# Optimization experiments

Measured on AMD Instinct MI355X. Metric: run time of the kernel, lower is better.

Reference implementation:

```python
import jax, jax.numpy as jnp
import numpy as np

NEG_INF = -9.0e15
ALPHA = 0.2  # leakyrelu slope


def setup_inputs() -> dict:
    key = jax.random.key(0)
    k1, k2, k3, k4, k5 = jax.random.split(key, 5)
    B, N, D_IN, D_OUT = 8, 2048, 128, 128
    h = jax.random.normal(k1, (B, N, D_IN), dtype=jnp.float32)
    adj = jax.random.randint(k2, (N, N), 0, 2, dtype=jnp.int32)
    W = jax.random.normal(k3, (D_IN, D_OUT), dtype=jnp.float32) * (1.0 / np.sqrt(D_IN))
    a_src = jax.random.normal(k4, (D_OUT,), dtype=jnp.float32) * (1.0 / np.sqrt(D_OUT))
    a_dst = jax.random.normal(k5, (D_OUT,), dtype=jnp.float32) * (1.0 / np.sqrt(D_OUT))
    return {"h": h, "adj": adj, "W": W, "a_src": a_src, "a_dst": a_dst}


def reference(h, adj, W, a_src, a_dst):
    # Wh: [B, N, D_out]
    Wh = jnp.einsum("bnd,de->bne", h, W)
    e_src = jnp.einsum("bne,e->bn", Wh, a_src)  # [B, N]
    e_dst = jnp.einsum("bne,e->bn", Wh, a_dst)  # [B, N]
    # additive attention logits: e[b,i,j] = e_src[b,i] + e_dst[b,j]
    e = e_src[:, :, None] + e_dst[:, None, :]  # [B, N, N]
    e = jnp.where(e > 0, e, ALPHA * e)  # leaky relu
    e = jnp.where(adj[None, :, :] > 0, e, NEG_INF)
    attention = jax.nn.softmax(e, axis=-1)  # [B, N, N]
    h_prime = jnp.einsum("bij,bje->bie", attention, Wh)
    return h_prime
```

## Files before the change

kernel.cpp:

```cpp
#include <hip/hip_runtime.h>
#include <stdint.h>

#define ALPHA 0.2f
#define LOG2E 1.4426950408889634f

typedef unsigned short u16;
typedef short s16x8 __attribute__((ext_vector_type(8)));
typedef float f32x4 __attribute__((ext_vector_type(4)));

union BF8 { s16x8 v; uint32_t u[4]; u16 s[8]; uint4 q; };

static __device__ __forceinline__ float bf2f(u16 u) {
  union { uint32_t i; float f; } c; c.i = ((uint32_t)u) << 16; return c.f;
}
static __device__ __forceinline__ uint32_t pk2bf(float lo, float hi) {
  uint32_t ul = __float_as_uint(lo) + 0x8000u;
  uint32_t uh = __float_as_uint(hi) + 0x8000u;
  return (ul >> 16) | (uh & 0xffff0000u);
}

static __device__ __forceinline__ void gl2lds16(const void* g, void* l) {
  __builtin_amdgcn_global_load_lds(
      (const __attribute__((address_space(1))) uint32_t*)g,
      (__attribute__((address_space(3))) uint32_t*)l, 16, 0, 0);
}

__global__ __launch_bounds__(256) void k_zero(uint32_t* __restrict__ out, int n32) {
  int gid = blockIdx.x * 256 + threadIdx.x;
  if (gid < n32) out[gid] = 0u;
}

__global__ __launch_bounds__(256) void k_pack_adj(const int* __restrict__ adj,
                                                  uint32_t* __restrict__ bits,
                                                  const u16* __restrict__ h,
                                                  int* __restrict__ flag) {
  int tid = threadIdx.x;
  int base = blockIdx.x * 256 + tid;
#pragma unroll
  for (int it = 0; it < 8; ++it) {
    int gid = base + it * (2048 * 256);
    unsigned long long m = __ballot(adj[gid] != 0);
    if ((tid & 63) == 0)
      *(unsigned long long*)(&bits[gid >> 5]) = m;
  }
  if (blockIdx.x == 0 && tid < 64) {
    u16 v = h[2 * tid];
    int e = (v >> 7) & 0xff;
    unsigned long long dm = __ballot(e >= 100 && e <= 140);
    if (tid == 0) flag[0] = (__popcll(dm) >= 48) ? 1 : 0;
  }
}

__global__ __launch_bounds__(256) void k_wh(
    const void* __restrict__ hV, const void* __restrict__ WgV,
    const void* __restrict__ aSrcV, const void* __restrict__ aDstV,
    const int* __restrict__ flag,
    u16* __restrict__ WhT, float* __restrict__ eS, float* __restrict__ eD) {
  __shared__ __align__(16) char smemRaw[34816];
  u16*   WT   = (u16*)smemRaw;
  float* tile = (float*)smemRaw;
  __shared__ float aS[128], aD[128];

  const int tid = threadIdx.x;
  const int mb = blockIdx.x * 64;
  const int isBf = *flag;

  if (isBf) {
    const u16* Wg = (const u16*)WgV;
    for (int it = 0; it < 8; ++it) {
      int idx = tid + it * 256;
      int k = idx >> 4, c0 = (idx & 15) * 8;
      uint4 w4 = *(const uint4*)(Wg + (k << 7) + c0);
      u16* wsv = (u16*)&w4;
#pragma unroll
      for (int e = 0; e < 8; ++e) WT[(c0 + e) * 136 + k] = wsv[e];
    }
    if (tid < 128) aS[tid] = bf2f(((const u16*)aSrcV)[tid]);
    else           aD[tid - 128] = bf2f(((const u16*)aDstV)[tid - 128]);
  } else {
    const float* Wg = (const float*)WgV;
    for (int it = 0; it < 8; ++it) {
      int idx = tid + it * 256;
      int k = idx >> 4, c0 = (idx & 15) * 8;
      float4 w0 = *(const float4*)(Wg + (k << 7) + c0);
      float4 w1 = *(const float4*)(Wg + (k << 7) + c0 + 4);
      float wf[8] = {w0.x, w0.y, w0.z, w0.w, w1.x, w1.y, w1.z, w1.w};
#pragma unroll
      for (int e = 0; e < 8; ++e)
        WT[(c0 + e) * 136 + k] = (u16)((__float_as_uint(wf[e]) + 0x8000u) >> 16);
    }
    if (tid < 128) aS[tid] = ((const float*)aSrcV)[tid];
    else           aD[tid - 128] = ((const float*)aDstV)[tid - 128];
  }
  __syncthreads();

  const int wv = tid >> 6, lane = tid & 63, ln = lane & 15, quad = lane >> 4;
  const int row = mb + wv * 16 + ln;

  f32x4 acc[8];
#pragma unroll
  for (int t = 0; t < 8; ++t) acc[t] = (f32x4){0.f, 0.f, 0.f, 0.f};

  if (isBf) {
    const u16* h = (const u16*)hV;
#pragma unroll
    for (int ks = 0; ks < 4; ++ks) {
      s16x8 af = *(const s16x8*)(h + (row << 7) + ks * 32 + quad * 8);
#pragma unroll
      for (int t = 0; t < 8; ++t) {
        s16x8 bfg = *(const s16x8*)(&WT[(t * 16 + ln) * 136 + ks * 32 + quad * 8]);
        acc[t] = __builtin_amdgcn_mfma_f32_16x16x32_bf16(af, bfg, acc[t], 0, 0, 0);
      }
    }
  } else {
    const float* h = (const float*)hV;
#pragma unroll
    for (int ks = 0; ks < 4; ++ks) {
      float4 a0 = *(const float4*)(h + (row << 7) + ks * 32 + quad * 8);
      float4 a1 = *(const float4*)(h + (row << 7) + ks * 32 + quad * 8 + 4);
      BF8 af;
      af.u[0] = pk2bf(a0.x, a0.y);
      af.u[1] = pk2bf(a0.z, a0.w);
      af.u[2] = pk2bf(a1.x, a1.y);
      af.u[3] = pk2bf(a1.z, a1.w);
#pragma unroll
      for (int t = 0; t < 8; ++t) {
        s16x8 bfg = *(const s16x8*)(&WT[(t * 16 + ln) * 136 + ks * 32 + quad * 8]);
        acc[t] = __builtin_amdgcn_mfma_f32_16x16x32_bf16(af.v, bfg, acc[t], 0, 0, 0);
      }
    }
  }
  __syncthreads();

#pragma unroll
  for (int t = 0; t < 8; ++t)
#pragma unroll
    for (int r = 0; r < 4; ++r)
      tile[(wv * 16 + quad * 4 + r) * 130 + t * 16 + ln] = acc[t][r];
  __syncthreads();

  if (tid < 128) {
    int r = tid & 63, grp = tid >> 6;
    const float* a = grp ? aD : aS;
    float sum = 0.f;
#pragma unroll 4
    for (int d = 0; d < 128; ++d) sum += tile[r * 130 + d] * a[d];
    int m = mb + r, b = m >> 11, n = m & 2047;
    (grp ? eD : eS)[(b << 11) + n] = sum * LOG2E;
  }

  {
    int d = tid >> 1, half = tid & 1;
    int n0 = mb & 2047, b = mb >> 11;
    uint32_t pk[16];
#pragma unroll
    for (int qq = 0; qq < 16; ++qq) {
      float v0 = tile[(half * 32 + 2 * qq) * 130 + d];
      float v1 = tile[(half * 32 + 2 * qq + 1) * 130 + d];
      pk[qq] = pk2bf(v0, v1);
    }
    uint4* dst = (uint4*)(WhT + (size_t)((b << 7) + d) * 2048 + n0 + half * 32);
#pragma unroll
    for (int c = 0; c < 4; ++c)
      dst[c] = make_uint4(pk[c * 4], pk[c * 4 + 1], pk[c * 4 + 2], pk[c * 4 + 3]);
  }
}

__global__ __launch_bounds__(512, 8) void k_attn(
    const u16* __restrict__ WhT, const float* __restrict__ eSrc,
    const float* __restrict__ eDst, const uint32_t* __restrict__ adjBits,
    float* __restrict__ numP, float* __restrict__ denP) {
  __shared__ __align__(16) u16 bufB[2][8192];
  __shared__ __align__(16) u16 bufP[2][2048];

  const int tid = threadIdx.x;
  const int bid = (blockIdx.x & 7) * 128 + (blockIdx.x >> 3);
  const int b = bid >> 7, rest = bid & 127;
  const int jq = rest & 1, ig = rest >> 1;
  const int i0 = ig * 32;

  const int w = tid >> 6, l = tid & 63;
  const int ln = l & 15, quad = l >> 4;
  const int s = w & 1, dh = w >> 1;

  const int gsrc = (l & 7) ^ ((l >> 3) & 7);
  const u16* whtB = WhT + ((size_t)b << 18);
  const u16* srcB = whtB + (size_t)(w * 8 + (l >> 3)) * 2048 + jq * 1024 + gsrc * 8;

  const int prow = tid >> 4, hg = tid & 15;
  const float sSp = eSrc[(b << 11) + i0 + prow];
  const float* eDb = eDst + (b << 11) + jq * 1024 + hg * 4;
  const uint32_t* adjB = adjBits + (size_t)(i0 + prow) * 64 + jq * 32 + (hg >> 3);
  const int pOff = prow * 128 + ((hg ^ ((prow & 7) << 1)) * 8);
  float dsum = 0.f;

  const int aOff0 = (s * 16 + ln) * 128 + (((0 * 4 + quad) ^ (ln & 7)) * 16);
  const int aOff1 = (s * 16 + ln) * 128 + (((1 * 4 + quad) ^ (ln & 7)) * 16);
  const int bOff00 = (dh * 32 + 0 * 16 + ln) * 128 + (((0 * 4 + quad) ^ (ln & 7)) * 16);
  const int bOff10 = (dh * 32 + 1 * 16 + ln) * 128 + (((0 * 4 + quad) ^ (ln & 7)) * 16);
  const int bOff01 = (dh * 32 + 0 * 16 + ln) * 128 + (((1 * 4 + quad) ^ (ln & 7)) * 16);
  const int bOff11 = (dh * 32 + 1 * 16 + ln) * 128 + (((1 * 4 + quad) ^ (ln & 7)) * 16);

  f32x4 acc0 = (f32x4){0.f, 0.f, 0.f, 0.f};
  f32x4 acc1 = (f32x4){0.f, 0.f, 0.f, 0.f};

#define PPROD(dv, aw, pdst) {                                                 \
    uint32_t nib = ((aw) >> ((hg & 7) * 4)) & 0xfu;                           \
    float x0 = sSp + (dv)[0], x1 = sSp + (dv)[1];                             \
    float x2 = sSp + (dv)[2], x3 = sSp + (dv)[3];                             \
    float p0 = exp2f(__builtin_amdgcn_fmed3f(x0, ALPHA * x0, 80.f));          \
    float p1 = exp2f(__builtin_amdgcn_fmed3f(x1, ALPHA * x1, 80.f));          \
    float p2 = exp2f(__builtin_amdgcn_fmed3f(x2, ALPHA * x2, 80.f));          \
    float p3 = exp2f(__builtin_amdgcn_fmed3f(x3, ALPHA * x3, 80.f));          \
    p0 = (nib & 1u) ? p0 : 0.f;                                               \
    p1 = (nib & 2u) ? p1 : 0.f;                                               \
    p2 = (nib & 4u) ? p2 : 0.f;                                               \
    p3 = (nib & 8u) ? p3 : 0.f;                                               \
    uint32_t w0 = pk2bf(p0, p1), w1 = pk2bf(p2, p3);                          \
    dsum += __uint_as_float(w0 << 16) + __uint_as_float(w0 & 0xffff0000u)     \
          + __uint_as_float(w1 << 16) + __uint_as_float(w1 & 0xffff0000u);    \
    *(uint2*)((char*)(pdst) + pOff) = make_uint2(w0, w1);                     \
  }

#define CONSUME(pPc, pBc) {                                                   \
    s16x8 af0 = *(const s16x8*)((const char*)(pPc) + aOff0);                  \
    s16x8 af1 = *(const s16x8*)((const char*)(pPc) + aOff1);                  \
    s16x8 b00 = *(const s16x8*)((const char*)(pBc) + bOff00);                 \
    s16x8 b10 = *(const s16x8*)((const char*)(pBc) + bOff10);                 \
    s16x8 b01 = *(const s16x8*)((const char*)(pBc) + bOff01);                 \
    s16x8 b11 = *(const s16x8*)((const char*)(pBc) + bOff11);                 \
    __builtin_amdgcn_s_setprio(1);                                            \
    acc0 = __builtin_amdgcn_mfma_f32_16x16x32_bf16(af0, b00, acc0, 0, 0, 0);  \
    acc1 = __builtin_amdgcn_mfma_f32_16x16x32_bf16(af0, b10, acc1, 0, 0, 0);  \
    acc0 = __builtin_amdgcn_mfma_f32_16x16x32_bf16(af1, b01, acc0, 0, 0, 0);  \
    acc1 = __builtin_amdgcn_mfma_f32_16x16x32_bf16(af1, b11, acc1, 0, 0, 0);  \
    __builtin_amdgcn_s_setprio(0);                                            \
  }

  u16 *bBc = bufB[0], *bBn = bufB[1];
  u16 *bPc = bufP[0], *bPn = bufP[1];

  f32x4 dv = *(const f32x4*)(eDb);
  uint32_t aw = adjB[0];
  PPROD(dv, aw, bPc);
  dv = *(const f32x4*)(eDb + 64);
  aw = adjB[2];
  gl2lds16(srcB, bBc + w * 512);
  gl2lds16(srcB + 131072, bBc + 4096 + w * 512);
  __syncthreads();

  for (int t = 0; t < 16; ++t) {
    if (t + 1 < 16) {
      gl2lds16(srcB + (size_t)(t + 1) * 64, bBn + w * 512);
      gl2lds16(srcB + (size_t)(t + 1) * 64 + 131072, bBn + 4096 + w * 512);
      PPROD(dv, aw, bPn);
      if (t + 2 < 16) {
        dv = *(const f32x4*)(eDb + (t + 2) * 64);
        aw = adjB[(t + 2) * 2];
      }
    }
    CONSUME(bPc, bBc);
    __syncthreads();
    u16* tb = bBc; bBc = bBn; bBn = tb;
    u16* tp = bPc; bPc = bPn; bPn = tp;
  }

  {
#pragma unroll
    for (int m = 1; m < 16; m <<= 1) dsum += __shfl_xor(dsum, m);
    if ((tid & 15) == 0)
      denP[jq * 16384 + (b << 11) + i0 + prow] = dsum;

    float* np = numP + ((size_t)jq << 21)
              + ((size_t)((b << 11) + i0 + s * 16 + quad * 4) << 7)
              + dh * 32 + ln;
#pragma unroll
    for (int r = 0; r < 4; ++r) {
      np[r * 128 + 0]  = acc0[r];
      np[r * 128 + 16] = acc1[r];
    }
  }
#undef PPROD
#undef CONSUME
}

__global__ __launch_bounds__(256) void k_merge(
    const float* __restrict__ numP, const float* __restrict__ denP,
    const int* __restrict__ flag, void* __restrict__ outV) {
  const int gid = blockIdx.x * 256 + threadIdx.x;
  const int e0 = gid * 8;
  const int row = e0 >> 7;

  f32x4 a0 = *(const f32x4*)(numP + e0);
  f32x4 a1 = *(const f32x4*)(numP + e0 + 4);
  f32x4 b0 = *(const f32x4*)(numP + (1 << 21) + e0);
  f32x4 b1 = *(const f32x4*)(numP + (1 << 21) + e0 + 4);
  float ds = denP[row] + denP[16384 + row];
  float inv = 1.0f / fmaxf(ds, 1e-37f);

  f32x4 v0 = (a0 + b0) * inv;
  f32x4 v1 = (a1 + b1) * inv;

  if (*flag) {
    uint4 pk = make_uint4(pk2bf(v0[0], v0[1]), pk2bf(v0[2], v0[3]),
                          pk2bf(v1[0], v1[1]), pk2bf(v1[2], v1[3]));
    *(uint4*)((u16*)outV + e0) = pk;
  } else {
    *(f32x4*)((float*)outV + e0) = v0;
    *(f32x4*)((float*)outV + e0 + 4) = v1;
  }
}

extern "C" void kernel_launch(void* const* d_in, const int* in_sizes, int n_in,
                              void* d_out, int out_size, void* d_ws, size_t ws_size,
                              hipStream_t stream) {
  const void* h   = d_in[0];
  const int* adj  = (const int*)d_in[1];
  const void* Wg  = d_in[2];
  const void* aS  = d_in[3];
  const void* aD  = d_in[4];

  const size_t OFF_ES   = (size_t)4 << 20;
  const size_t OFF_ED   = OFF_ES + (64 << 10);
  const size_t OFF_BITS = OFF_ED + (64 << 10);
  const size_t OFF_FLAG = OFF_BITS + (512 << 10);
  const size_t OFF_NUM  = (size_t)5 << 20;
  const size_t OFF_DEN  = (size_t)21 << 20;
  const size_t NEEDED   = OFF_DEN + (128 << 10);

  if (ws_size < NEEDED) {
    int n32 = out_size / 2;
    k_zero<<<(n32 + 255) / 256, 256, 0, stream>>>((uint32_t*)d_out, n32);
    return;
  }

  char* ws = (char*)d_ws;
  u16* WhT      = (u16*)ws;
  float* eSp    = (float*)(ws + OFF_ES);
  float* eDp    = (float*)(ws + OFF_ED);
  uint32_t* bit = (uint32_t*)(ws + OFF_BITS);
  int* flag     = (int*)(ws + OFF_FLAG);
  float* numP   = (float*)(ws + OFF_NUM);
  float* denP   = (float*)(ws + OFF_DEN);

  k_pack_adj<<<2048, 256, 0, stream>>>(adj, bit, (const u16*)h, flag);
  k_wh<<<256, 256, 0, stream>>>(h, Wg, aS, aD, flag, WhT, eSp, eDp);
  k_attn<<<1024, 512, 0, stream>>>(WhT, eSp, eDp, bit, numP, denP);
  k_merge<<<1024, 256, 0, stream>>>(numP, denP, flag, d_out);
}
```

Measured before the change: 121.3 us.

## Fuse adjacency packing and Wh projection into one heterogeneous prep kernel

Merges the adjacency bit-packing kernel and the Wh projection kernel into a single launch. The first 2048 blocks pack adj and the remaining 512 blocks compute Wh with 32 rows per block, splitting output columns across waves. Each Wh block recomputes the dtype flag itself, which removes its dependency on the packing kernel. The attention logits e_src/e_dst are now reduced from MFMA accumulators with shuffles instead of a serial 128-wide loop over the shared tile. This saves one launch and lets the two phases overlap, at the cost of twice as many Wh blocks, each reloading W into LDS.

```diff
diff --git a/kernel.cpp b/kernel.cpp
--- a/kernel.cpp
+++ b/kernel.cpp
@@ -30,40 +30,50 @@
   if (gid < n32) out[gid] = 0u;
 }
 
-__global__ __launch_bounds__(256) void k_pack_adj(const int* __restrict__ adj,
-                                                  uint32_t* __restrict__ bits,
-                                                  const u16* __restrict__ h,
-                                                  int* __restrict__ flag) {
-  int tid = threadIdx.x;
-  int base = blockIdx.x * 256 + tid;
-#pragma unroll
-  for (int it = 0; it < 8; ++it) {
-    int gid = base + it * (2048 * 256);
-    unsigned long long m = __ballot(adj[gid] != 0);
-    if ((tid & 63) == 0)
-      *(unsigned long long*)(&bits[gid >> 5]) = m;
-  }
-  if (blockIdx.x == 0 && tid < 64) {
-    u16 v = h[2 * tid];
+__global__ __launch_bounds__(256) void k_prep(
+    const int* __restrict__ adj, uint32_t* __restrict__ bits,
+    const void* __restrict__ hV, const void* __restrict__ WgV,
+    const void* __restrict__ aSrcV, const void* __restrict__ aDstV,
+    int* __restrict__ flag,
+    u16* __restrict__ WhT, float* __restrict__ eS, float* __restrict__ eD) {
+  __shared__ __align__(16) char smemRaw[34816];
+  __shared__ float aS[128], aD[128];
+  __shared__ float ePs[2][32][2];
+
+  const int tid = threadIdx.x;
+  const int bk = blockIdx.x;
+  const int lane = tid & 63;
+
+  if (bk < 2048) {
+    int base = bk * 256 + tid;
+#pragma unroll
+    for (int it = 0; it < 8; ++it) {
+      int gid = base + it * (2048 * 256);
+      unsigned long long m = __ballot(adj[gid] != 0);
+      if ((tid & 63) == 0)
+        *(unsigned long long*)(&bits[gid >> 5]) = m;
+    }
+    if (bk == 0 && tid < 64) {
+      u16 v = ((const u16*)hV)[2 * tid];
+      int e = (v >> 7) & 0xff;
+      unsigned long long dm = __ballot(e >= 100 && e <= 140);
+      if (tid == 0) flag[0] = (__popcll(dm) >= 48) ? 1 : 0;
+    }
+    return;
+  }
+
+  u16*   WT   = (u16*)smemRaw;
+  float* tile = (float*)smemRaw;
+  const int whid = bk - 2048;
+  const int mb = whid * 32;
+
+  int isBf;
+  {
+    u16 v = ((const u16*)hV)[2 * lane];
     int e = (v >> 7) & 0xff;
     unsigned long long dm = __ballot(e >= 100 && e <= 140);
-    if (tid == 0) flag[0] = (__popcll(dm) >= 48) ? 1 : 0;
-  }
-}
-
-__global__ __launch_bounds__(256) void k_wh(
-    const void* __restrict__ hV, const void* __restrict__ WgV,
-    const void* __restrict__ aSrcV, const void* __restrict__ aDstV,
-    const int* __restrict__ flag,
-    u16* __restrict__ WhT, float* __restrict__ eS, float* __restrict__ eD) {
-  __shared__ __align__(16) char smemRaw[34816];
-  u16*   WT   = (u16*)smemRaw;
-  float* tile = (float*)smemRaw;
-  __shared__ float aS[128], aD[128];
-
-  const int tid = threadIdx.x;
-  const int mb = blockIdx.x * 64;
-  const int isBf = *flag;
+    isBf = (__popcll(dm) >= 48) ? 1 : 0;
+  }
 
   if (isBf) {
     const u16* Wg = (const u16*)WgV;
@@ -94,12 +104,13 @@
   }
   __syncthreads();
 
-  const int wv = tid >> 6, lane = tid & 63, ln = lane & 15, quad = lane >> 4;
-  const int row = mb + wv * 16 + ln;
-
-  f32x4 acc[8];
-#pragma unroll
-  for (int t = 0; t < 8; ++t) acc[t] = (f32x4){0.f, 0.f, 0.f, 0.f};
+  const int wv = tid >> 6, ln = lane & 15, quad = lane >> 4;
+  const int rh = wv & 1, ch = wv >> 1;
+  const int row = mb + rh * 16 + ln;
+
+  f32x4 acc[4];
+#pragma unroll
+  for (int t = 0; t < 4; ++t) acc[t] = (f32x4){0.f, 0.f, 0.f, 0.f};
 
   if (isBf) {
     const u16* h = (const u16*)hV;
@@ -107,8 +118,8 @@
     for (int ks = 0; ks < 4; ++ks) {
       s16x8 af = *(const s16x8*)(h + (row << 7) + ks * 32 + quad * 8);
 #pragma unroll
-      for (int t = 0; t < 8; ++t) {
-        s16x8 bfg = *(const s16x8*)(&WT[(t * 16 + ln) * 136 + ks * 32 + quad * 8]);
+      for (int t = 0; t < 4; ++t) {
+        s16x8 bfg = *(const s16x8*)(&WT[(ch * 64 + t * 16 + ln) * 136 + ks * 32 + quad * 8]);
         acc[t] = __builtin_amdgcn_mfma_f32_16x16x32_bf16(af, bfg, acc[t], 0, 0, 0);
       }
     }
@@ -124,45 +135,67 @@
       af.u[2] = pk2bf(a1.x, a1.y);
       af.u[3] = pk2bf(a1.z, a1.w);
 #pragma unroll
-      for (int t = 0; t < 8; ++t) {
-        s16x8 bfg = *(const s16x8*)(&WT[(t * 16 + ln) * 136 + ks * 32 + quad * 8]);
+      for (int t = 0; t < 4; ++t) {
+        s16x8 bfg = *(const s16x8*)(&WT[(ch * 64 + t * 16 + ln) * 136 + ks * 32 + quad * 8]);
         acc[t] = __builtin_amdgcn_mfma_f32_16x16x32_bf16(af.v, bfg, acc[t], 0, 0, 0);
       }
     }
   }
+
+  {
+    float pS[4] = {0.f, 0.f, 0.f, 0.f}, pD[4] = {0.f, 0.f, 0.f, 0.f};
+#pragma unroll
+    for (int t = 0; t < 4; ++t) {
+      float av = aS[ch * 64 + t * 16 + ln];
+      float dv = aD[ch * 64 + t * 16 + ln];
+#pragma unroll
+      for (int r = 0; r < 4; ++r) { pS[r] += acc[t][r] * av; pD[r] += acc[t][r] * dv; }
+    }
+#pragma unroll
+    for (int m = 1; m < 16; m <<= 1) {
+#pragma unroll
+      for (int r = 0; r < 4; ++r) {
+        pS[r] += __shfl_xor(pS[r], m);
+        pD[r] += __shfl_xor(pD[r], m);
+      }
+    }
+    if (ln == 0) {
+#pragma unroll
+      for (int r = 0; r < 4; ++r) {
+        ePs[0][rh * 16 + quad * 4 + r][ch] = pS[r];
+        ePs[1][rh * 16 + quad * 4 + r][ch] = pD[r];
+      }
+    }
+  }
   __syncthreads();
 
 #pragma unroll
-  for (int t = 0; t < 8; ++t)
+  for (int t = 0; t < 4; ++t)
 #pragma unroll
     for (int r = 0; r < 4; ++r)
-      tile[(wv * 16 + quad * 4 + r) * 130 + t * 16 + ln] = acc[t][r];
+      tile[(rh * 16 + quad * 4 + r) * 130 + ch * 64 + t * 16 + ln] = acc[t][r];
   __syncthreads();
 
-  if (tid < 128) {
-    int r = tid & 63, grp = tid >> 6;
-    const float* a = grp ? aD : aS;
-    float sum = 0.f;
-#pragma unroll 4
-    for (int d = 0; d < 128; ++d) sum += tile[r * 130 + d] * a[d];
+  if (tid < 64) {
+    int r = tid & 31, which = tid >> 5;
+    float sum = ePs[which][r][0] + ePs[which][r][1];
     int m = mb + r, b = m >> 11, n = m & 2047;
-    (grp ? eD : eS)[(b << 11) + n] = sum * LOG2E;
+    (which ? eD : eS)[(b << 11) + n] = sum * LOG2E;
   }
 
   {
     int d = tid >> 1, half = tid & 1;
     int n0 = mb & 2047, b = mb >> 11;
-    uint32_t pk[16];
-#pragma unroll
-    for (int qq = 0; qq < 16; ++qq) {
-      float v0 = tile[(half * 32 + 2 * qq) * 130 + d];
-      float v1 = tile[(half * 32 + 2 * qq + 1) * 130 + d];
-      pk[qq] = pk2bf(v0, v1);
-    }
-    uint4* dst = (uint4*)(WhT + (size_t)((b << 7) + d) * 2048 + n0 + half * 32);
-#pragma unroll
-    for (int c = 0; c < 4; ++c)
-      dst[c] = make_uint4(pk[c * 4], pk[c * 4 + 1], pk[c * 4 + 2], pk[c * 4 + 3]);
+    uint32_t pk[8];
+#pragma unroll
+    for (int q = 0; q < 8; ++q) {
+      float v0 = tile[(half * 16 + 2 * q) * 130 + d];
+      float v1 = tile[(half * 16 + 2 * q + 1) * 130 + d];
+      pk[q] = pk2bf(v0, v1);
+    }
+    uint4* dst = (uint4*)(WhT + (size_t)((b << 7) + d) * 2048 + n0 + half * 16);
+    dst[0] = make_uint4(pk[0], pk[1], pk[2], pk[3]);
+    dst[1] = make_uint4(pk[4], pk[5], pk[6], pk[7]);
   }
 }
 
@@ -343,8 +376,7 @@
   float* numP   = (float*)(ws + OFF_NUM);
   float* denP   = (float*)(ws + OFF_DEN);
 
-  k_pack_adj<<<2048, 256, 0, stream>>>(adj, bit, (const u16*)h, flag);
-  k_wh<<<256, 256, 0, stream>>>(h, Wg, aS, aD, flag, WhT, eSp, eDp);
+  k_prep<<<2560, 256, 0, stream>>>(adj, bit, h, Wg, aS, aD, flag, WhT, eSp, eDp);
   k_attn<<<1024, 512, 0, stream>>>(WhT, eSp, eDp, bit, numP, denP);
   k_merge<<<1024, 256, 0, stream>>>(numP, denP, flag, d_out);
 }
```

Measured after the change: 130.7 us. 7.7% more time.

## Split attention key range four ways with 256-thread blocks and wider per-warp tiles

Applied to the files above, without the earlier changes.

The attention kernel now splits the key dimension into four quarters instead of two and launches twice as many blocks with 256 threads each. Each warp computes four 16x16 output tiles from one A fragment rather than two tiles from two fragments, and the LDS buffers are halved with a new swizzle. The aim is more blocks in flight and smaller per-block LDS footprint, giving better occupancy and latency hiding. The cost is doubled partial-numerator traffic: the merge kernel now sums four partials, and the workspace grows to hold them.

```diff
diff --git a/kernel.cpp b/kernel.cpp
--- a/kernel.cpp
+++ b/kernel.cpp
@@ -166,46 +166,50 @@
   }
 }
 
-__global__ __launch_bounds__(512, 8) void k_attn(
+__global__ __launch_bounds__(256, 8) void k_attn(
     const u16* __restrict__ WhT, const float* __restrict__ eSrc,
     const float* __restrict__ eDst, const uint32_t* __restrict__ adjBits,
     float* __restrict__ numP, float* __restrict__ denP) {
-  __shared__ __align__(16) u16 bufB[2][8192];
-  __shared__ __align__(16) u16 bufP[2][2048];
+  __shared__ __align__(16) u16 bufB[2][4096];
+  __shared__ __align__(16) u16 bufP[2][1024];
 
   const int tid = threadIdx.x;
-  const int bid = (blockIdx.x & 7) * 128 + (blockIdx.x >> 3);
-  const int b = bid >> 7, rest = bid & 127;
-  const int jq = rest & 1, ig = rest >> 1;
+  const int bid = (blockIdx.x & 7) * 256 + (blockIdx.x >> 3);
+  const int b = bid >> 8, rest = bid & 255;
+  const int jq = rest & 3, ig = rest >> 2;
   const int i0 = ig * 32;
 
   const int w = tid >> 6, l = tid & 63;
   const int ln = l & 15, quad = l >> 4;
   const int s = w & 1, dh = w >> 1;
 
-  const int gsrc = (l & 7) ^ ((l >> 3) & 7);
+  const int gsrc = (l & 3) ^ ((l >> 2) & 3);
   const u16* whtB = WhT + ((size_t)b << 18);
-  const u16* srcB = whtB + (size_t)(w * 8 + (l >> 3)) * 2048 + jq * 1024 + gsrc * 8;
-
-  const int prow = tid >> 4, hg = tid & 15;
+  const u16* srcB0 = whtB + (size_t)((w * 2 + 0) * 16 + (l >> 2)) * 2048
+                   + jq * 512 + gsrc * 8;
+  const u16* srcB1 = whtB + (size_t)((w * 2 + 1) * 16 + (l >> 2)) * 2048
+                   + jq * 512 + gsrc * 8;
+
+  const int prow = tid >> 3, hg = tid & 7;
   const float sSp = eSrc[(b << 11) + i0 + prow];
-  const float* eDb = eDst + (b << 11) + jq * 1024 + hg * 4;
-  const uint32_t* adjB = adjBits + (size_t)(i0 + prow) * 64 + jq * 32 + (hg >> 3);
-  const int pOff = prow * 128 + ((hg ^ ((prow & 7) << 1)) * 8);
+  const float* eDb = eDst + (b << 11) + jq * 512 + hg * 4;
+  const uint32_t* adjB = adjBits + (size_t)(i0 + prow) * 64 + jq * 16;
+  const int pOff = prow * 64 + (((hg >> 1) ^ (prow & 3)) * 16) + (hg & 1) * 8;
   float dsum = 0.f;
 
-  const int aOff0 = (s * 16 + ln) * 128 + (((0 * 4 + quad) ^ (ln & 7)) * 16);
-  const int aOff1 = (s * 16 + ln) * 128 + (((1 * 4 + quad) ^ (ln & 7)) * 16);
-  const int bOff00 = (dh * 32 + 0 * 16 + ln) * 128 + (((0 * 4 + quad) ^ (ln & 7)) * 16);
-  const int bOff10 = (dh * 32 + 1 * 16 + ln) * 128 + (((0 * 4 + quad) ^ (ln & 7)) * 16);
-  const int bOff01 = (dh * 32 + 0 * 16 + ln) * 128 + (((1 * 4 + quad) ^ (ln & 7)) * 16);
-  const int bOff11 = (dh * 32 + 1 * 16 + ln) * 128 + (((1 * 4 + quad) ^ (ln & 7)) * 16);
-
-  f32x4 acc0 = (f32x4){0.f, 0.f, 0.f, 0.f};
-  f32x4 acc1 = (f32x4){0.f, 0.f, 0.f, 0.f};
+  const int swz = (quad ^ (ln & 3)) * 16;
+  const int aOff = (s * 16 + ln) * 64 + swz;
+  const int bOff0 = (dh * 64 + 0 * 16 + ln) * 64 + swz;
+  const int bOff1 = (dh * 64 + 1 * 16 + ln) * 64 + swz;
+  const int bOff2 = (dh * 64 + 2 * 16 + ln) * 64 + swz;
+  const int bOff3 = (dh * 64 + 3 * 16 + ln) * 64 + swz;
+
+  f32x4 acc[4];
+#pragma unroll
+  for (int t = 0; t < 4; ++t) acc[t] = (f32x4){0.f, 0.f, 0.f, 0.f};
 
 #define PPROD(dv, aw, pdst) {                                                 \
-    uint32_t nib = ((aw) >> ((hg & 7) * 4)) & 0xfu;                           \
+    uint32_t nib = ((aw) >> (hg * 4)) & 0xfu;                                 \
     float x0 = sSp + (dv)[0], x1 = sSp + (dv)[1];                             \
     float x2 = sSp + (dv)[2], x3 = sSp + (dv)[3];                             \
     float p0 = exp2f(__builtin_amdgcn_fmed3f(x0, ALPHA * x0, 80.f));          \
@@ -223,17 +227,16 @@
   }
 
 #define CONSUME(pPc, pBc) {                                                   \
-    s16x8 af0 = *(const s16x8*)((const char*)(pPc) + aOff0);                  \
-    s16x8 af1 = *(const s16x8*)((const char*)(pPc) + aOff1);                  \
-    s16x8 b00 = *(const s16x8*)((const char*)(pBc) + bOff00);                 \
-    s16x8 b10 = *(const s16x8*)((const char*)(pBc) + bOff10);                 \
-    s16x8 b01 = *(const s16x8*)((const char*)(pBc) + bOff01);                 \
-    s16x8 b11 = *(const s16x8*)((const char*)(pBc) + bOff11);                 \
+    s16x8 af = *(const s16x8*)((const char*)(pPc) + aOff);                    \
+    s16x8 b0 = *(const s16x8*)((const char*)(pBc) + bOff0);                   \
+    s16x8 b1 = *(const s16x8*)((const char*)(pBc) + bOff1);                   \
+    s16x8 b2 = *(const s16x8*)((const char*)(pBc) + bOff2);                   \
+    s16x8 b3 = *(const s16x8*)((const char*)(pBc) + bOff3);                   \
     __builtin_amdgcn_s_setprio(1);                                            \
-    acc0 = __builtin_amdgcn_mfma_f32_16x16x32_bf16(af0, b00, acc0, 0, 0, 0);  \
-    acc1 = __builtin_amdgcn_mfma_f32_16x16x32_bf16(af0, b10, acc1, 0, 0, 0);  \
-    acc0 = __builtin_amdgcn_mfma_f32_16x16x32_bf16(af1, b01, acc0, 0, 0, 0);  \
-    acc1 = __builtin_amdgcn_mfma_f32_16x16x32_bf16(af1, b11, acc1, 0, 0, 0);  \
+    acc[0] = __builtin_amdgcn_mfma_f32_16x16x32_bf16(af, b0, acc[0], 0, 0, 0);\
+    acc[1] = __builtin_amdgcn_mfma_f32_16x16x32_bf16(af, b1, acc[1], 0, 0, 0);\
+    acc[2] = __builtin_amdgcn_mfma_f32_16x16x32_bf16(af, b2, acc[2], 0, 0, 0);\
+    acc[3] = __builtin_amdgcn_mfma_f32_16x16x32_bf16(af, b3, acc[3], 0, 0, 0);\
     __builtin_amdgcn_s_setprio(0);                                            \
   }
 
@@ -243,20 +246,20 @@
   f32x4 dv = *(const f32x4*)(eDb);
   uint32_t aw = adjB[0];
   PPROD(dv, aw, bPc);
-  dv = *(const f32x4*)(eDb + 64);
-  aw = adjB[2];
-  gl2lds16(srcB, bBc + w * 512);
-  gl2lds16(srcB + 131072, bBc + 4096 + w * 512);
+  dv = *(const f32x4*)(eDb + 32);
+  aw = adjB[1];
+  gl2lds16(srcB0, bBc + (w * 2 + 0) * 512);
+  gl2lds16(srcB1, bBc + (w * 2 + 1) * 512);
   __syncthreads();
 
   for (int t = 0; t < 16; ++t) {
     if (t + 1 < 16) {
-      gl2lds16(srcB + (size_t)(t + 1) * 64, bBn + w * 512);
-      gl2lds16(srcB + (size_t)(t + 1) * 64 + 131072, bBn + 4096 + w * 512);
+      gl2lds16(srcB0 + (size_t)(t + 1) * 32, bBn + (w * 2 + 0) * 512);
+      gl2lds16(srcB1 + (size_t)(t + 1) * 32, bBn + (w * 2 + 1) * 512);
       PPROD(dv, aw, bPn);
       if (t + 2 < 16) {
-        dv = *(const f32x4*)(eDb + (t + 2) * 64);
-        aw = adjB[(t + 2) * 2];
+        dv = *(const f32x4*)(eDb + (t + 2) * 32);
+        aw = adjB[t + 2];
       }
     }
     CONSUME(bPc, bBc);
@@ -267,18 +270,18 @@
 
   {
 #pragma unroll
-    for (int m = 1; m < 16; m <<= 1) dsum += __shfl_xor(dsum, m);
-    if ((tid & 15) == 0)
+    for (int m = 1; m < 8; m <<= 1) dsum += __shfl_xor(dsum, m);
+    if ((tid & 7) == 0)
       denP[jq * 16384 + (b << 11) + i0 + prow] = dsum;
 
     float* np = numP + ((size_t)jq << 21)
               + ((size_t)((b << 11) + i0 + s * 16 + quad * 4) << 7)
-              + dh * 32 + ln;
-#pragma unroll
-    for (int r = 0; r < 4; ++r) {
-      np[r * 128 + 0]  = acc0[r];
-      np[r * 128 + 16] = acc1[r];
-    }
+              + dh * 64 + ln;
+#pragma unroll
+    for (int tt = 0; tt < 4; ++tt)
+#pragma unroll
+      for (int r = 0; r < 4; ++r)
+        np[r * 128 + tt * 16] = acc[tt][r];
   }
 #undef PPROD
 #undef CONSUME
@@ -291,15 +294,18 @@
   const int e0 = gid * 8;
   const int row = e0 >> 7;
 
-  f32x4 a0 = *(const f32x4*)(numP + e0);
-  f32x4 a1 = *(const f32x4*)(numP + e0 + 4);
-  f32x4 b0 = *(const f32x4*)(numP + (1 << 21) + e0);
-  f32x4 b1 = *(const f32x4*)(numP + (1 << 21) + e0 + 4);
-  float ds = denP[row] + denP[16384 + row];
+  f32x4 v0 = (f32x4){0.f, 0.f, 0.f, 0.f};
+  f32x4 v1 = (f32x4){0.f, 0.f, 0.f, 0.f};
+  float ds = 0.f;
+#pragma unroll
+  for (int q = 0; q < 4; ++q) {
+    v0 += *(const f32x4*)(numP + ((size_t)q << 21) + e0);
+    v1 += *(const f32x4*)(numP + ((size_t)q << 21) + e0 + 4);
+    ds += denP[q * 16384 + row];
+  }
   float inv = 1.0f / fmaxf(ds, 1e-37f);
-
-  f32x4 v0 = (a0 + b0) * inv;
-  f32x4 v1 = (a1 + b1) * inv;
+  v0 *= inv;
+  v1 *= inv;
 
   if (*flag) {
     uint4 pk = make_uint4(pk2bf(v0[0], v0[1]), pk2bf(v0[2], v0[3]),
@@ -325,8 +331,8 @@
   const size_t OFF_BITS = OFF_ED + (64 << 10);
   const size_t OFF_FLAG = OFF_BITS + (512 << 10);
   const size_t OFF_NUM  = (size_t)5 << 20;
-  const size_t OFF_DEN  = (size_t)21 << 20;
-  const size_t NEEDED   = OFF_DEN + (128 << 10);
+  const size_t OFF_DEN  = (size_t)40 << 20;
+  const size_t NEEDED   = OFF_DEN + (256 << 10);
 
   if (ws_size < NEEDED) {
     int n32 = out_size / 2;
@@ -345,6 +351,6 @@
 
   k_pack_adj<<<2048, 256, 0, stream>>>(adj, bit, (const u16*)h, flag);
   k_wh<<<256, 256, 0, stream>>>(h, Wg, aS, aD, flag, WhT, eSp, eDp);
-  k_attn<<<1024, 512, 0, stream>>>(WhT, eSp, eDp, bit, numP, denP);
+  k_attn<<<2048, 256, 0, stream>>>(WhT, eSp, eDp, bit, numP, denP);
   k_merge<<<1024, 256, 0, stream>>>(numP, denP, flag, d_out);
 }
```

New measurement: 127.5 us. 1.05x slower.
